# Performance work log

Hardware: AMD Instinct MI355X
Metric: run time of the kernel (lower is better)

## Reference

```python
import jax, jax.numpy as jnp
import numpy as np
import math

EMB = 1024
H = 8          # num_heads
HD = EMB // H // 2  # head_dim = 64
LAMBDA_INIT = 0.8
B, N = 2, 2048


def setup_inputs() -> dict:
    key = jax.random.key(0)
    ks = jax.random.split(key, 16)
    s = 1.0 / math.sqrt(EMB)
    d = {
        'q': jax.random.normal(ks[0], (B, N, EMB), jnp.float32),
        'k': jax.random.normal(ks[1], (B, N, EMB), jnp.float32),
        'v': jax.random.normal(ks[2], (B, N, EMB), jnp.float32),
        'Wq': jax.random.uniform(ks[3], (EMB, EMB), jnp.float32, -s, s),
        'bq': jax.random.uniform(ks[4], (EMB,), jnp.float32, -s, s),
        'Wk': jax.random.uniform(ks[5], (EMB, EMB), jnp.float32, -s, s),
        'bk': jax.random.uniform(ks[6], (EMB,), jnp.float32, -s, s),
        'Wv': jax.random.uniform(ks[7], (EMB, EMB), jnp.float32, -s, s),
        'bv': jax.random.uniform(ks[8], (EMB,), jnp.float32, -s, s),
        'Wo': jax.random.uniform(ks[9], (EMB, EMB), jnp.float32, -s, s),
        'bo': jax.random.uniform(ks[10], (EMB,), jnp.float32, -s, s),
        'lambda_q1': 0.1 * jax.random.normal(ks[11], (HD,), jnp.float32),
        'lambda_k1': 0.1 * jax.random.normal(ks[12], (HD,), jnp.float32),
        'lambda_q2': 0.1 * jax.random.normal(ks[13], (HD,), jnp.float32),
        'lambda_k2': 0.1 * jax.random.normal(ks[14], (HD,), jnp.float32),
    }
    return d


def reference(q, k, v, Wq, bq, Wk, bk, Wv, bv, Wo, bo,
              lambda_q1, lambda_k1, lambda_q2, lambda_k2):
    b, n, _ = q.shape
    # projections (torch Linear: x @ W.T + b)
    qp = q @ Wq.T + bq            # [b, n, EMB]
    kp = k @ Wk.T + bk
    vp = v @ Wv.T + bv
    # split into 2*H sub-heads of width HD for q/k; H heads of width 2*HD for v
    qh = qp.reshape(b, n, 2 * H, HD).transpose(0, 2, 1, 3)   # [b, 2H, n, HD]
    kh = kp.reshape(b, n, 2 * H, HD).transpose(0, 2, 1, 3)   # [b, 2H, n, HD]
    vh = vp.reshape(b, n, H, 2 * HD).transpose(0, 2, 1, 3)   # [b, H, n, 2HD]
    scale = 1.0 / math.sqrt(HD)
    attn = jnp.einsum('bhqd,bhkd->bhqk', qh, kh) * scale      # [b, 2H, n, n]
    attn = jax.nn.softmax(attn, axis=-1)
    lam1 = jnp.exp(jnp.sum(lambda_q1 * lambda_k1))
    lam2 = jnp.exp(jnp.sum(lambda_q2 * lambda_k2))
    lam = lam1 - lam2 + LAMBDA_INIT
    attn = attn.reshape(b, H, 2, n, n)
    diff = attn[:, :, 0] - lam * attn[:, :, 1]                # [b, H, n, n]
    out = jnp.einsum('bhqk,bhkd->bhqd', diff, vh)             # [b, H, n, 2HD]
    out = out.transpose(0, 2, 1, 3).reshape(b, n, H * 2 * HD)
    return out @ Wo.T + bo
```

## Files before the change

kernel.cpp:

```cpp
#include <hip/hip_runtime.h>
#include <stdint.h>


typedef __attribute__((ext_vector_type(8))) __bf16 bf16x8;
typedef __attribute__((ext_vector_type(4))) __bf16 bf16x4;
typedef __attribute__((ext_vector_type(4))) float f32x4;
typedef __attribute__((ext_vector_type(16))) float f32x16;
typedef __attribute__((ext_vector_type(8))) unsigned short u16x8;
typedef __attribute__((ext_vector_type(4))) unsigned short u16x4;
typedef __attribute__((ext_vector_type(4))) unsigned int u32x4;
typedef unsigned short u16;
typedef unsigned int u32;

#define EMB 1024
#define NSEQ 2048
#define NBATCH 2
#define NHEAD 8
#define MROWS (NBATCH*NSEQ)
#define QSCALE 0.18033688011112042f

__device__ __forceinline__ u16x4 pk4(float a, float b, float c, float d){
  bf16x4 h; h[0]=(__bf16)a; h[1]=(__bf16)b; h[2]=(__bf16)c; h[3]=(__bf16)d;
  return __builtin_bit_cast(u16x4, h);
}
__device__ __forceinline__ u16 bf1(float f){
  __bf16 h = (__bf16)f; return __builtin_bit_cast(unsigned short, h);
}
__device__ __forceinline__ u32 cvtpk(float lo, float hi){
  u32 r; asm("v_cvt_pk_bf16_f32 %0, %1, %2" : "=v"(r) : "v"(lo), "v"(hi)); return r;
}

__device__ __forceinline__ bf16x8 ld8(const u16* p){
  return __builtin_bit_cast(bf16x8, *(const u16x8*)p);
}

__device__ __forceinline__ void glds16(const u16* g, u16* l){
  __builtin_amdgcn_global_load_lds(
      (const __attribute__((address_space(1))) u32*)g,
      (__attribute__((address_space(3))) u32*)l, 16, 0, 0);
}

__global__ void cvt_k(const float* __restrict__ q, const float* __restrict__ k,
                      const float* __restrict__ v, const float* __restrict__ Wq,
                      const float* __restrict__ Wk, const float* __restrict__ Wv,
                      const float* __restrict__ Wo,
                      const float* __restrict__ lq1, const float* __restrict__ lk1,
                      const float* __restrict__ lq2, const float* __restrict__ lk2,
                      u16* qb, u16* kb, u16* vb, u16* Wqb, u16* Wkb, u16* Wvb, u16* Wob,
                      float* lam)
{
  if (blockIdx.x == 0 && threadIdx.x < 64){
    int l = threadIdx.x;
    float p1 = lq1[l]*lk1[l];
    float p2 = lq2[l]*lk2[l];
    #pragma unroll
    for (int m=1; m<64; m<<=1){ p1 += __shfl_xor(p1, m, 64); p2 += __shfl_xor(p2, m, 64); }
    if (l==0) lam[0] = __expf(p1) - __expf(p2) + 0.8f;
  }
  const int NQ4 = (NBATCH*NSEQ*EMB)/4;
  const int NW4 = (EMB*EMB)/4;
  const int total = 3*NQ4 + 4*NW4;
  for (int i = blockIdx.x*blockDim.x + threadIdx.x; i < total; i += gridDim.x*blockDim.x){
    const float* src; u16* dst; int off;
    if (i < 3*NQ4){
      int t = i / NQ4; off = i - t*NQ4;
      src = t==0 ? q : (t==1 ? k : v);
      dst = t==0 ? qb : (t==1 ? kb : vb);
    } else {
      int j = i - 3*NQ4;
      int t = j / NW4; off = j - t*NW4;
      src = t==0 ? Wq : (t==1 ? Wk : (t==2 ? Wv : Wo));
      dst = t==0 ? Wqb : (t==1 ? Wkb : (t==2 ? Wvb : Wob));
    }
    f32x4 f = *((const f32x4*)src + off);
    *((u16x4*)dst + off) = pk4(f[0], f[1], f[2], f[3]);
  }
}

__device__ __forceinline__ void gemm_core(
    const u16* __restrict__ A, const u16* __restrict__ W, const float* __restrict__ bias,
    u16* __restrict__ Ybf, u16* __restrict__ Yvt, int mode,
    float oscale, int m0, int n0, u16* As, u16* Bs)
{
  const int tid = threadIdx.x, w = tid >> 6, l = tid & 63;
  const int l15 = l & 15, lg = l >> 4;
  const int wr = w >> 1, wc = w & 1;
  const int srow = w*16 + (l >> 2);
  const int skel = (l & 3) * 8;

  f32x4 acc[4][4] = {};

  for (int kt = 0; kt < EMB/32; ++kt){
    const int kb = kt*32 + skel;
    glds16(A + (size_t)(m0 + srow)*EMB + kb,      As + w*512);
    glds16(A + (size_t)(m0 + 64 + srow)*EMB + kb, As + 2048 + w*512);
    glds16(W + (size_t)(n0 + srow)*EMB + kb,      Bs + w*512);
    glds16(W + (size_t)(n0 + 64 + srow)*EMB + kb, Bs + 2048 + w*512);
    __syncthreads();

    bf16x8 af[4], bfr[4];
    #pragma unroll
    for (int mi=0; mi<4; ++mi) af[mi]  = ld8(As + (wr*64 + mi*16 + l15)*32 + lg*8);
    #pragma unroll
    for (int ni=0; ni<4; ++ni) bfr[ni] = ld8(Bs + (wc*64 + ni*16 + l15)*32 + lg*8);
    #pragma unroll
    for (int mi=0; mi<4; ++mi)
      #pragma unroll
      for (int ni=0; ni<4; ++ni)
        acc[mi][ni] = __builtin_amdgcn_mfma_f32_16x16x32_bf16(af[mi], bfr[ni], acc[mi][ni], 0,0,0);
    __syncthreads();
  }

  #pragma unroll
  for (int mi=0; mi<4; ++mi){
    const int mr = m0 + wr*64 + mi*16 + lg*4;
    #pragma unroll
    for (int ni=0; ni<4; ++ni){
      const int nc = n0 + wc*64 + ni*16 + l15;
      const float bvs = bias[nc]*oscale;
      if (mode == 0){
        #pragma unroll
        for (int i=0;i<4;++i) Ybf[(size_t)(mr+i)*EMB + nc] = bf1(fmaf(acc[mi][ni][i], oscale, bvs));
      } else {
        const int h = nc >> 7, vd = nc & 127, bb = mr >> 11, t = mr & 2047;
        u16x4 pkv = pk4(acc[mi][ni][0]+bvs, acc[mi][ni][1]+bvs,
                        acc[mi][ni][2]+bvs, acc[mi][ni][3]+bvs);
        *(u16x4*)(Yvt + ((size_t)((bb*NHEAD + h)*128 + vd))*NSEQ + t) = pkv;
      }
    }
  }
}

__global__ __launch_bounds__(256) void gemm_qkv(
    const u16* qb, const u16* kb, const u16* vb,
    const u16* Wqb, const u16* Wkb, const u16* Wvb,
    const float* bq, const float* bk, const float* bv,
    u16* Qp, u16* Kp, u16* Vt)
{
  __shared__ __align__(16) u16 As[4096], Bs[4096];
  const int bid = blockIdx.x;
  const int c = bid & 7, slot = bid >> 3;
  const int g = c + 8*(slot >> 3);
  const int x = slot & 7;
  const int y = g & 31, z = g >> 5;
  const int m0 = y*128, n0 = x*128;

  const u16* A = z==0 ? qb : (z==1 ? kb : vb);
  const u16* W = z==0 ? Wqb : (z==1 ? Wkb : Wvb);
  const float* bias = z==0 ? bq : (z==1 ? bk : bv);
  if (z == 0)      gemm_core(A, W, bias, Qp, nullptr, 0, QSCALE, m0, n0, As, Bs);
  else if (z == 1) gemm_core(A, W, bias, Kp, nullptr, 0, 1.0f,  m0, n0, As, Bs);
  else             gemm_core(A, W, bias, nullptr, Vt, 1, 1.0f,  m0, n0, As, Bs);
}

__global__ __launch_bounds__(256) void gemm_out_k(
    const u16* __restrict__ Xc, const u16* __restrict__ Wob,
    const float* __restrict__ bo, float* __restrict__ out)
{
  __shared__ __align__(16) u16 As[2048], Bs[4096];
  const int tid = threadIdx.x, w = tid >> 6, l = tid & 63;
  const int l15 = l & 15, lg = l >> 4;
  const int bid = blockIdx.x;
  const int c = bid & 7, slot = bid >> 3;
  const int gy = c + 8*(slot >> 3);
  const int x = slot & 7;
  const int m0 = gy*64, n0 = x*128;
  const int wr = w >> 1, wc = w & 1;
  const int srow = w*16 + (l >> 2);
  const int skel = (l & 3) * 8;

  f32x4 acc[2][4] = {};

  for (int kt = 0; kt < EMB/32; ++kt){
    const int kb = kt*32 + skel;
    glds16(Xc  + (size_t)(m0 + srow)*EMB + kb,      As + w*512);
    glds16(Wob + (size_t)(n0 + srow)*EMB + kb,      Bs + w*512);
    glds16(Wob + (size_t)(n0 + 64 + srow)*EMB + kb, Bs + 2048 + w*512);
    __syncthreads();

    bf16x8 af[2], bfr[4];
    #pragma unroll
    for (int mi=0; mi<2; ++mi) af[mi]  = ld8(As + (wr*32 + mi*16 + l15)*32 + lg*8);
    #pragma unroll
    for (int ni=0; ni<4; ++ni) bfr[ni] = ld8(Bs + (wc*64 + ni*16 + l15)*32 + lg*8);
    #pragma unroll
    for (int mi=0; mi<2; ++mi)
      #pragma unroll
      for (int ni=0; ni<4; ++ni)
        acc[mi][ni] = __builtin_amdgcn_mfma_f32_16x16x32_bf16(af[mi], bfr[ni], acc[mi][ni], 0,0,0);
    __syncthreads();
  }

  #pragma unroll
  for (int mi=0; mi<2; ++mi){
    const int mr = m0 + wr*32 + mi*16 + lg*4;
    #pragma unroll
    for (int ni=0; ni<4; ++ni){
      const int nc = n0 + wc*64 + ni*16 + l15;
      const float bv = bo[nc];
      #pragma unroll
      for (int i=0;i<4;++i) out[(size_t)(mr+i)*EMB + nc] = acc[mi][ni][i] + bv;
    }
  }
}

__global__ __launch_bounds__(512, 4) void attn_k(
    const u16* __restrict__ Qp, const u16* __restrict__ Kp,
    const u16* __restrict__ Vt, const float* __restrict__ lamp,
    u16* __restrict__ Xc)
{
  __shared__ __align__(16) char shm[66560];
  u16* ldsK = (u16*)shm;
  u16* ldsV = (u16*)(shm + 32768);

  const int tid = threadIdx.x, w = tid >> 6, l = tid & 63;
  const int l31 = l & 31, hl = l >> 5;
  const int qg = w & 1, s = (w >> 1) & 1, g = w >> 2;
  const int wg = w & 3;
  int bid = blockIdx.x;
  bid = (bid & 7)*64 + (bid >> 3);
  const int qt = bid & 31, bh = bid >> 5;
  const int b = bh >> 3, h = bh & 7;
  const int q0 = qt*64 + qg*32;

  const u16* Kg = Kp + ((size_t)b*NSEQ)*EMB + h*128;
  const u16* Vg = Vt + ((size_t)((b*NHEAD + h)*128))*NSEQ;

  const u16* qbase = Qp + (size_t)(b*NSEQ + q0 + l31)*EMB + (2*h + s)*64;
  bf16x8 qa[4];
  #pragma unroll
  for (int ks=0; ks<4; ++ks) qa[ks] = ld8(qbase + ks*16 + hl*8);

  f32x16 acc[4] = {};
  float l_run = 0.f;

  auto STAGE = [&](int buf, int t){
    const u16* kg = Kg + (size_t)t*32*EMB;
    u16* kd = ldsK + (g*2 + buf)*4096;
    #pragma unroll
    for (int j=0;j<2;++j){
      int row = wg*8 + j*4 + (l >> 4);
      glds16(kg + (size_t)row*EMB + (((l&15) ^ (row&15))*8), kd + (wg*8 + j*4)*128);
    }
    const u16* vg = Vg + t*32;
    u16* vd2 = ldsV + (g*2 + buf)*4096;
    #pragma unroll
    for (int j=0;j<2;++j){
      int row = wg*32 + j*16 + (l >> 2);
      glds16(vg + (size_t)row*NSEQ + (((l&3) ^ ((row>>1)&3))*8), vd2 + (wg*32 + j*16)*32);
    }
  };

  auto BODY = [&](const u16* Kb, const u16* Vb){
    f32x16 st = {};
    __builtin_amdgcn_s_setprio(1);
    #pragma unroll
    for (int ks=0; ks<4; ++ks){
      int c = s*8 + ks*2 + hl;
      bf16x8 kf = ld8(Kb + l31*128 + ((c ^ (l31&15))*8));
      st = __builtin_amdgcn_mfma_f32_32x32x16_bf16(kf, qa[ks], st, 0,0,0);
    }
    __builtin_amdgcn_s_setprio(0);

    float p[16];
    #pragma unroll
    for (int r=0; r<16; ++r) p[r] = exp2f(st[r]);
    float s0 = (p[0]+p[1]) + (p[2]+p[3]);
    float s1 = (p[4]+p[5]) + (p[6]+p[7]);
    float s2 = (p[8]+p[9]) + (p[10]+p[11]);
    float s3 = (p[12]+p[13]) + (p[14]+p[15]);
    float ssum = (s0+s1) + (s2+s3);
    ssum += __shfl_xor(ssum, 32, 64);
    l_run += ssum;

    bf16x8 pa[2];
    #pragma unroll
    for (int kb=0; kb<2; ++kb){
      u32 w0 = cvtpk(p[8*kb+0], p[8*kb+1]);
      u32 w1 = cvtpk(p[8*kb+2], p[8*kb+3]);
      u32 w2 = cvtpk(p[8*kb+4], p[8*kb+5]);
      u32 w3 = cvtpk(p[8*kb+6], p[8*kb+7]);
      asm volatile("v_permlane32_swap_b32 %0, %1" : "+v"(w0), "+v"(w2));
      asm volatile("v_permlane32_swap_b32 %0, %1" : "+v"(w1), "+v"(w3));
      u32x4 t4; t4[0]=w0; t4[1]=w1; t4[2]=w2; t4[3]=w3;
      pa[kb] = __builtin_bit_cast(bf16x8, t4);
    }

    __builtin_amdgcn_s_setprio(1);
    #pragma unroll
    for (int kb=0; kb<2; ++kb)
      #pragma unroll
      for (int v=0; v<4; ++v){
        int row = v*32 + l31;
        int kc = kb*2 + hl;
        bf16x8 vf = ld8(Vb + row*32 + ((kc ^ ((row>>1)&3))*8));
        acc[v] = __builtin_amdgcn_mfma_f32_32x32x16_bf16(vf, pa[kb], acc[v], 0,0,0);
      }
    __builtin_amdgcn_s_setprio(0);
  };

  const u16* Kb0 = ldsK + (g*2 + 0)*4096;  const u16* Vb0 = ldsV + (g*2 + 0)*4096;
  const u16* Kb1 = ldsK + (g*2 + 1)*4096;  const u16* Vb1 = ldsV + (g*2 + 1)*4096;

  STAGE(0, g);
  __syncthreads();

  for (int jj = 0; jj < 16; ++jj){
    STAGE(1, 2*(2*jj+1) + g);
    BODY(Kb0, Vb0);
    __syncthreads();
    if (jj < 15) STAGE(0, 2*(2*jj+2) + g);
    BODY(Kb1, Vb1);
    __syncthreads();
  }

  float* pool = (float*)shm;
  float* lsh  = (float*)(shm + 65536);
  const int slot = qg*2 + s;

  if (g == 1){
    #pragma unroll
    for (int v=0; v<4; ++v)
      #pragma unroll
      for (int rr=0; rr<4; ++rr){
        f32x4 t4; t4[0]=acc[v][rr*4+0]; t4[1]=acc[v][rr*4+1];
        t4[2]=acc[v][rr*4+2]; t4[3]=acc[v][rr*4+3];
        *(f32x4*)(pool + (((slot*4 + v)*4 + rr)*64 + l)*4) = t4;
      }
    if (hl == 0) lsh[slot*32 + l31] = l_run;
  }
  __syncthreads();
  float L = 1.f;
  if (g == 0){
    L = l_run + lsh[slot*32 + l31];
    #pragma unroll
    for (int v=0; v<4; ++v)
      #pragma unroll
      for (int rr=0; rr<4; ++rr){
        f32x4 c = *(f32x4*)(pool + (((slot*4 + v)*4 + rr)*64 + l)*4);
        #pragma unroll
        for (int e=0; e<4; ++e) acc[v][rr*4+e] += c[e];
      }
  }
  __syncthreads();
  if (g == 0 && s == 1){
    const float f = lamp[0] / L;
    #pragma unroll
    for (int v=0; v<4; ++v)
      #pragma unroll
      for (int rr=0; rr<4; ++rr){
        f32x4 t4; t4[0]=acc[v][rr*4+0]*f; t4[1]=acc[v][rr*4+1]*f;
        t4[2]=acc[v][rr*4+2]*f; t4[3]=acc[v][rr*4+3]*f;
        *(f32x4*)(pool + (((qg*4 + v)*4 + rr)*64 + l)*4) = t4;
      }
  }
  __syncthreads();
  if (g == 0 && s == 0){
    const float i0 = 1.f / L;
    #pragma unroll
    for (int v=0; v<4; ++v)
      #pragma unroll
      for (int rr=0; rr<4; ++rr){
        f32x4 c = *(f32x4*)(pool + (((qg*4 + v)*4 + rr)*64 + l)*4);
        u16x4 o = pk4(acc[v][rr*4+0]*i0 - c[0], acc[v][rr*4+1]*i0 - c[1],
                      acc[v][rr*4+2]*i0 - c[2], acc[v][rr*4+3]*i0 - c[3]);
        const int col = v*32 + rr*8 + hl*4;
        *(u16x4*)(Xc + (size_t)(b*NSEQ + q0 + l31)*EMB + h*128 + col) = o;
      }
  }
}

extern "C" void kernel_launch(void* const* d_in, const int* in_sizes, int n_in,
                              void* d_out, int out_size, void* d_ws, size_t ws_size,
                              hipStream_t stream)
{
  const float* q   = (const float*)d_in[0];
  const float* k   = (const float*)d_in[1];
  const float* v   = (const float*)d_in[2];
  const float* Wq  = (const float*)d_in[3];
  const float* bq  = (const float*)d_in[4];
  const float* Wk  = (const float*)d_in[5];
  const float* bk  = (const float*)d_in[6];
  const float* Wv  = (const float*)d_in[7];
  const float* bv  = (const float*)d_in[8];
  const float* Wo  = (const float*)d_in[9];
  const float* bo  = (const float*)d_in[10];
  const float* lq1 = (const float*)d_in[11];
  const float* lk1 = (const float*)d_in[12];
  const float* lq2 = (const float*)d_in[13];
  const float* lk2 = (const float*)d_in[14];

  const size_t NQ = (size_t)MROWS*EMB;
  const size_t NW = (size_t)EMB*EMB;
  u16* qb  = (u16*)d_ws;
  u16* kb  = qb + NQ;
  u16* vb  = kb + NQ;
  u16* Wqb = vb + NQ;
  u16* Wkb = Wqb + NW;
  u16* Wvb = Wkb + NW;
  u16* Wob = Wvb + NW;
  u16* Qp  = Wob + NW;
  u16* Kp  = Qp + NQ;
  u16* Vt  = Kp + NQ;
  u16* Xc  = Vt + NQ;
  float* lam = (float*)(Xc + NQ);

  cvt_k<<<2048, 256, 0, stream>>>(q, k, v, Wq, Wk, Wv, Wo,
                                  lq1, lk1, lq2, lk2,
                                  qb, kb, vb, Wqb, Wkb, Wvb, Wob, lam);
  gemm_qkv<<<768, 256, 0, stream>>>(
      qb, kb, vb, Wqb, Wkb, Wvb, bq, bk, bv, Qp, Kp, Vt);
  attn_k<<<dim3(NBATCH*NHEAD*(NSEQ/64)), 512, 0, stream>>>(Qp, Kp, Vt, lam, Xc);
  gemm_out_k<<<512, 256, 0, stream>>>(Xc, Wob, bo, (float*)d_out);
}
```

Before: 145.5 us.

## Double GEMM K-tile to 64 and XOR-swizzle LDS rows to avoid bank conflicts

Both the QKV projection GEMM and the output projection GEMM now stage 64-wide K slices per iteration instead of 32, which halves the number of loop iterations and block barriers. Shared-memory tiles are laid out with an XOR swizzle of the 16-byte chunk index by row, and the fragment reads apply the same swizzle. This is meant to avoid LDS bank conflicts that the wider 128-byte rows would otherwise cause. The cost is double the LDS footprint per block, which may reduce occupancy.

New measurement: 149.9 us. 1.03x slower.

```diff
diff --git a/kernel.cpp b/kernel.cpp
--- a/kernel.cpp
+++ b/kernel.cpp
@@ -85,29 +85,41 @@
   const int tid = threadIdx.x, w = tid >> 6, l = tid & 63;
   const int l15 = l & 15, lg = l >> 4;
   const int wr = w >> 1, wc = w & 1;
-  const int srow = w*16 + (l >> 2);
-  const int skel = (l & 3) * 8;
+  const int sr8 = l >> 3;
+  const int sps = l & 7;
 
   f32x4 acc[4][4] = {};
 
-  for (int kt = 0; kt < EMB/32; ++kt){
-    const int kb = kt*32 + skel;
-    glds16(A + (size_t)(m0 + srow)*EMB + kb,      As + w*512);
-    glds16(A + (size_t)(m0 + 64 + srow)*EMB + kb, As + 2048 + w*512);
-    glds16(W + (size_t)(n0 + srow)*EMB + kb,      Bs + w*512);
-    glds16(W + (size_t)(n0 + 64 + srow)*EMB + kb, Bs + 2048 + w*512);
-    __syncthreads();
-
-    bf16x8 af[4], bfr[4];
-    #pragma unroll
-    for (int mi=0; mi<4; ++mi) af[mi]  = ld8(As + (wr*64 + mi*16 + l15)*32 + lg*8);
-    #pragma unroll
-    for (int ni=0; ni<4; ++ni) bfr[ni] = ld8(Bs + (wc*64 + ni*16 + l15)*32 + lg*8);
-    #pragma unroll
-    for (int mi=0; mi<4; ++mi)
-      #pragma unroll
-      for (int ni=0; ni<4; ++ni)
-        acc[mi][ni] = __builtin_amdgcn_mfma_f32_16x16x32_bf16(af[mi], bfr[ni], acc[mi][ni], 0,0,0);
+  for (int kt = 0; kt < EMB/64; ++kt){
+    const int kb = kt*64;
+    #pragma unroll
+    for (int j=0;j<4;++j){
+      const int row = w*32 + j*8 + sr8;
+      const int c = sps ^ (row & 7);
+      glds16(A + (size_t)(m0 + row)*EMB + kb + c*8, As + (w*32 + j*8)*64);
+      glds16(W + (size_t)(n0 + row)*EMB + kb + c*8, Bs + (w*32 + j*8)*64);
+    }
+    __syncthreads();
+
+    #pragma unroll
+    for (int ks=0; ks<2; ++ks){
+      bf16x8 af[4], bfr[4];
+      #pragma unroll
+      for (int mi=0; mi<4; ++mi){
+        const int row = wr*64 + mi*16 + l15;
+        af[mi] = ld8(As + row*64 + (((ks*4 + lg) ^ (row&7))*8));
+      }
+      #pragma unroll
+      for (int ni=0; ni<4; ++ni){
+        const int row = wc*64 + ni*16 + l15;
+        bfr[ni] = ld8(Bs + row*64 + (((ks*4 + lg) ^ (row&7))*8));
+      }
+      #pragma unroll
+      for (int mi=0; mi<4; ++mi)
+        #pragma unroll
+        for (int ni=0; ni<4; ++ni)
+          acc[mi][ni] = __builtin_amdgcn_mfma_f32_16x16x32_bf16(af[mi], bfr[ni], acc[mi][ni], 0,0,0);
+    }
     __syncthreads();
   }
 
@@ -137,7 +149,7 @@
     const float* bq, const float* bk, const float* bv,
     u16* Qp, u16* Kp, u16* Vt)
 {
-  __shared__ __align__(16) u16 As[4096], Bs[4096];
+  __shared__ __align__(16) u16 As[8192], Bs[8192];
   const int bid = blockIdx.x;
   const int c = bid & 7, slot = bid >> 3;
   const int g = c + 8*(slot >> 3);
@@ -157,7 +169,7 @@
     const u16* __restrict__ Xc, const u16* __restrict__ Wob,
     const float* __restrict__ bo, float* __restrict__ out)
 {
-  __shared__ __align__(16) u16 As[2048], Bs[4096];
+  __shared__ __align__(16) u16 As[4096], Bs[8192];
   const int tid = threadIdx.x, w = tid >> 6, l = tid & 63;
   const int l15 = l & 15, lg = l >> 4;
   const int bid = blockIdx.x;
@@ -166,28 +178,46 @@
   const int x = slot & 7;
   const int m0 = gy*64, n0 = x*128;
   const int wr = w >> 1, wc = w & 1;
-  const int srow = w*16 + (l >> 2);
-  const int skel = (l & 3) * 8;
+  const int sr8 = l >> 3;
+  const int sps = l & 7;
 
   f32x4 acc[2][4] = {};
 
-  for (int kt = 0; kt < EMB/32; ++kt){
-    const int kb = kt*32 + skel;
-    glds16(Xc  + (size_t)(m0 + srow)*EMB + kb,      As + w*512);
-    glds16(Wob + (size_t)(n0 + srow)*EMB + kb,      Bs + w*512);
-    glds16(Wob + (size_t)(n0 + 64 + srow)*EMB + kb, Bs + 2048 + w*512);
-    __syncthreads();
-
-    bf16x8 af[2], bfr[4];
-    #pragma unroll
-    for (int mi=0; mi<2; ++mi) af[mi]  = ld8(As + (wr*32 + mi*16 + l15)*32 + lg*8);
-    #pragma unroll
-    for (int ni=0; ni<4; ++ni) bfr[ni] = ld8(Bs + (wc*64 + ni*16 + l15)*32 + lg*8);
-    #pragma unroll
-    for (int mi=0; mi<2; ++mi)
-      #pragma unroll
-      for (int ni=0; ni<4; ++ni)
-        acc[mi][ni] = __builtin_amdgcn_mfma_f32_16x16x32_bf16(af[mi], bfr[ni], acc[mi][ni], 0,0,0);
+  for (int kt = 0; kt < EMB/64; ++kt){
+    const int kb = kt*64;
+    #pragma unroll
+    for (int j=0;j<2;++j){
+      const int row = w*16 + j*8 + sr8;
+      const int cc = sps ^ (row & 7);
+      glds16(Xc + (size_t)(m0 + row)*EMB + kb + cc*8, As + (w*16 + j*8)*64);
+    }
+    #pragma unroll
+    for (int j=0;j<4;++j){
+      const int row = w*32 + j*8 + sr8;
+      const int cc = sps ^ (row & 7);
+      glds16(Wob + (size_t)(n0 + row)*EMB + kb + cc*8, Bs + (w*32 + j*8)*64);
+    }
+    __syncthreads();
+
+    #pragma unroll
+    for (int ks=0; ks<2; ++ks){
+      bf16x8 af[2], bfr[4];
+      #pragma unroll
+      for (int mi=0; mi<2; ++mi){
+        const int row = wr*32 + mi*16 + l15;
+        af[mi] = ld8(As + row*64 + (((ks*4 + lg) ^ (row&7))*8));
+      }
+      #pragma unroll
+      for (int ni=0; ni<4; ++ni){
+        const int row = wc*64 + ni*16 + l15;
+        bfr[ni] = ld8(Bs + row*64 + (((ks*4 + lg) ^ (row&7))*8));
+      }
+      #pragma unroll
+      for (int mi=0; mi<2; ++mi)
+        #pragma unroll
+        for (int ni=0; ni<4; ++ni)
+          acc[mi][ni] = __builtin_amdgcn_mfma_f32_16x16x32_bf16(af[mi], bfr[ni], acc[mi][ni], 0,0,0);
+    }
     __syncthreads();
   }
 
```
